# Optimization experiments

Measured on AMD Instinct MI355X. Metric: run time of the kernel, lower is better.

## Reference

```python
import jax, jax.numpy as jnp
import numpy as np

D_MODEL = 1024
N_HEADS = 16
HEAD_DIM = D_MODEL // N_HEADS


def setup_inputs() -> dict:
    key = jax.random.key(0)
    k1, k2, k3 = jax.random.split(key, 3)
    x = jax.random.normal(k1, (4, 2048, D_MODEL), dtype=jnp.float32)
    # torch Linear weight is [out, in]; y = x @ W.T
    w_qkv = jax.random.normal(k2, (3 * D_MODEL, D_MODEL), dtype=jnp.float32) * (1.0 / np.sqrt(D_MODEL))
    w_proj = jax.random.normal(k3, (D_MODEL, D_MODEL), dtype=jnp.float32) * (1.0 / np.sqrt(D_MODEL))
    return {"x": x, "w_qkv": w_qkv, "w_proj": w_proj}


def reference(x, w_qkv, w_proj):
    B, T, C = x.shape
    qkv = jnp.einsum('btc,oc->bto', x, w_qkv)  # [B,T,3C]
    q, k, v = jnp.split(qkv, 3, axis=-1)
    # [B,T,H,D] -> [B,H,T,D]
    def to_heads(t):
        return t.reshape(B, T, N_HEADS, HEAD_DIM).transpose(0, 2, 1, 3)
    q, k, v = to_heads(q), to_heads(k), to_heads(v)
    scale = 1.0 / np.sqrt(HEAD_DIM).astype(np.float32)
    scores = jnp.einsum('bhqd,bhkd->bhqk', q, k) * scale  # [B,H,T,T]
    causal = jnp.tril(jnp.ones((T, T), dtype=bool))
    scores = jnp.where(causal, scores, jnp.finfo(scores.dtype).min)
    attn = jax.nn.softmax(scores, axis=-1)
    out = jnp.einsum('bhqk,bhkd->bhqd', attn, v)  # [B,H,T,D]
    out = out.transpose(0, 2, 1, 3).reshape(B, T, C)
    return jnp.einsum('btc,oc->bto', out, w_proj)
```

## Files before the change

kernel.cpp:

```cpp
#include <hip/hip_runtime.h>

#define B_ 4
#define T_ 2048
#define C_ 1024
#define H_ 16
#define D_ 64

typedef __bf16 bf16;
typedef bf16 bf16x8 __attribute__((ext_vector_type(8)));
typedef bf16 bf16x4v __attribute__((ext_vector_type(4)));
typedef float f32x4 __attribute__((ext_vector_type(4)));

__device__ __forceinline__ int probe_is_f32(const void* p, int lane) {
  float v = fminf(fabsf((float)((const bf16*)p)[lane]), 100.f);
#pragma unroll
  for (int o = 1; o < 64; o <<= 1) v += __shfl_xor(v, o, 64);
  return v > 300.f ? 1 : 0;
}

__device__ __forceinline__ void gload16(const void* g, void* l) {
  __builtin_amdgcn_global_load_lds(
      (const __attribute__((address_space(1))) void*)g,
      (__attribute__((address_space(3))) void*)l, 16, 0, 0);
}

__global__ __launch_bounds__(256) void cvt_bf16(const void* __restrict__ src,
                                                bf16* __restrict__ dst,
                                                int n8) {
  if (!probe_is_f32(src, threadIdx.x & 63)) return;
  int i = blockIdx.x * 256 + threadIdx.x;
  if (i >= n8) return;
  const float* s = (const float*)src + (size_t)i * 8;
  f32x4 u0 = *(const f32x4*)s;
  f32x4 u1 = *(const f32x4*)(s + 4);
  bf16x8 o;
#pragma unroll
  for (int j = 0; j < 4; ++j) { o[j] = (bf16)u0[j]; o[4 + j] = (bf16)u1[j]; }
  *(bf16x8*)(dst + (size_t)i * 8) = o;
}

__global__ __launch_bounds__(256, 3) void gemm_bt(
    const void* __restrict__ A, const void* __restrict__ W,
    const bf16* __restrict__ Wcvt, int M, int N, int K, int amode, int omode,
    void* __restrict__ out, bf16* __restrict__ qb, bf16* __restrict__ kb,
    bf16* __restrict__ vtb, const void* __restrict__ px,
    const void* __restrict__ pwq, const void* __restrict__ pwp, int bsel) {
  __shared__ __align__(16) char lds[24576];
  char* ldsA = lds;
  char* ldsB = lds + 16384;

  const int ntiles = N >> 7;
  const int tm = blockIdx.x / ntiles;
  const int tn = blockIdx.x % ntiles;
  const int tid = threadIdx.x;
  const int lane = tid & 63;
  const int wv = tid >> 6;
  const int wm = wv >> 1, wn = wv & 1;
  const int lm = lane & 15, lq = lane >> 4;

  const int fx = probe_is_f32(px, lane);
  const int fwq = probe_is_f32(pwq, lane);
  const int fwp = probe_is_f32(pwp, lane);
  const int outF32 = fx | fwq | fwp;
  const int aF32 = (amode == 0) ? fx : 0;
  const int bF32 = bsel ? fwp : fwq;
  const bf16* Wb = bF32 ? Wcvt : (const bf16*)W;

  size_t boff[2];
#pragma unroll
  for (int h = 0; h < 2; ++h) {
    int c = tid + h * 256, rbk = c >> 6, ll = c & 63;
    boff[h] = (size_t)(tn * 128 + rbk * 16 + (ll & 15)) * K + (ll >> 4) * 8;
  }
  size_t aofff[4];
  size_t aoffb[2];
  int ab2[2], at2[2], acq[2];
  if (aF32) {
#pragma unroll
    for (int h = 0; h < 4; ++h) {
      int c = tid + h * 256, rb = c >> 7, w = c & 127;
      int q = w >> 5, lmm = (w >> 1) & 15, hf = w & 1;
      aofff[h] = (size_t)(tm * 128 + rb * 16 + lmm) * K + q * 8 + hf * 4;
    }
  } else {
#pragma unroll
    for (int h = 0; h < 2; ++h) {
      int c = tid + h * 256, rbk = c >> 6, ll = c & 63;
      int row = tm * 128 + rbk * 16 + (ll & 15);
      aoffb[h] = (size_t)row * K + (ll >> 4) * 8;
      ab2[h] = row >> 11;
      at2[h] = row & 2047;
      acq[h] = ll >> 4;
    }
  }

  f32x4 acc[4][4] = {};

  for (int k0 = 0; k0 < K; k0 += 32) {
    __syncthreads();
    if (aF32) {
#pragma unroll
      for (int h = 0; h < 4; ++h)
        gload16((const float*)A + aofff[h] + k0, ldsA + (tid + h * 256) * 16);
    } else if (amode == 2) {
#pragma unroll
      for (int h = 0; h < 2; ++h) {
        int kk = k0 + acq[h] * 8;
        size_t off =
            ((size_t)(ab2[h] * H_ + (kk >> 6)) * T_ + at2[h]) * D_ + (kk & 63);
        gload16((const bf16*)A + off, ldsA + (tid + h * 256) * 16);
      }
    } else {
#pragma unroll
      for (int h = 0; h < 2; ++h)
        gload16((const bf16*)A + aoffb[h] + k0, ldsA + (tid + h * 256) * 16);
    }
#pragma unroll
    for (int h = 0; h < 2; ++h)
      gload16(Wb + boff[h] + k0, ldsB + (tid + h * 256) * 16);
    __syncthreads();

    bf16x8 af[4], bff[4];
    if (aF32) {
#pragma unroll
      for (int i = 0; i < 4; ++i) {
        const char* p = ldsA + (wm * 4 + i) * 2048 + lane * 32;
        f32x4 u0 = *(const f32x4*)p;
        f32x4 u1 = *(const f32x4*)(p + 16);
#pragma unroll
        for (int j = 0; j < 4; ++j) {
          af[i][j] = (bf16)u0[j];
          af[i][4 + j] = (bf16)u1[j];
        }
      }
    } else {
#pragma unroll
      for (int i = 0; i < 4; ++i)
        af[i] = *(const bf16x8*)(ldsA + (wm * 4 + i) * 1024 + lane * 16);
    }
#pragma unroll
    for (int j = 0; j < 4; ++j)
      bff[j] = *(const bf16x8*)(ldsB + (wn * 4 + j) * 1024 + lane * 16);
#pragma unroll
    for (int i = 0; i < 4; ++i)
#pragma unroll
      for (int j = 0; j < 4; ++j)
        acc[i][j] = __builtin_amdgcn_mfma_f32_16x16x32_bf16(af[i], bff[j],
                                                            acc[i][j], 0, 0, 0);
  }

  if (omode == 0) {
#pragma unroll
    for (int i = 0; i < 4; ++i) {
      int row0 = tm * 128 + wm * 64 + i * 16 + lq * 4;
#pragma unroll
      for (int j = 0; j < 4; ++j) {
        int col = tn * 128 + wn * 64 + j * 16 + lm;
#pragma unroll
        for (int r = 0; r < 4; ++r) {
          size_t idx = (size_t)(row0 + r) * N + col;
          if (outF32) ((float*)out)[idx] = acc[i][j][r];
          else        ((bf16*)out)[idx]  = (bf16)acc[i][j][r];
        }
      }
    }
  } else {
#pragma unroll
    for (int j = 0; j < 4; ++j) {
      int o = tn * 128 + wn * 64 + j * 16 + lm;
      int which = o >> 10;
      int c = o & 1023;
      int h = c >> 6, d = c & 63;
#pragma unroll
      for (int i = 0; i < 4; ++i) {
        int row0 = tm * 128 + wm * 64 + i * 16 + lq * 4;
        int b = row0 >> 11, t0 = row0 & 2047;
        if (which == 2) {
          bf16x4v pk;
#pragma unroll
          for (int r = 0; r < 4; ++r) pk[r] = (bf16)acc[i][j][r];
          *(bf16x4v*)(vtb + ((size_t)((b * H_ + h) * D_ + d)) * T_ + t0) = pk;
        } else {
          bf16* dst = (which == 0) ? qb : kb;
#pragma unroll
          for (int r = 0; r < 4; ++r)
            dst[((size_t)((b * H_ + h) * T_ + t0 + r)) * D_ + d] =
                (bf16)acc[i][j][r];
        }
      }
    }
  }
}

__global__ __launch_bounds__(256, 4) void attn_fwd(bf16* __restrict__ Q,
                                                   const bf16* __restrict__ Kk,
                                                   const bf16* __restrict__ Vt) {
  __shared__ __align__(16) char lds[12288];
  char* ldsK = lds;
  char* ldsV = lds + 4096;
  char* ldsP = lds + 8192;

  const int tid = threadIdx.x;
  const int bh = blockIdx.x & 63;
  const int qt = blockIdx.x >> 6;
  const int lane = tid & 63;
  const int wv = tid >> 6;
  const int lm = lane & 15, lq = lane >> 4;
  const int q0w = qt * 64 + wv * 16;

  bf16x8 qa[2];
  {
    const bf16* qbase = Q + ((size_t)(bh * T_ + q0w + lm)) * D_ + lq * 8;
    qa[0] = *(const bf16x8*)(qbase);
    qa[1] = *(const bf16x8*)(qbase + 32);
  }

  const int kRow = (wv >> 1) * 16 + lm;
  const int kD = (wv & 1) * 32 + lq * 8;
  const int vD = wv * 16 + lm;

  const bf16* ksrc = Kk + ((size_t)(bh * T_ + kRow)) * D_ + kD;
  const bf16* vsrc = Vt + ((size_t)(bh * D_ + vD)) * T_ + lq * 8;

  f32x4 oacc[4] = {};
  float lsum[4] = {0.f, 0.f, 0.f, 0.f};
  char* myP = ldsP + wv * 1024;
  const int jend = qt * 64 + 64;

  for (int j0 = 0; j0 < jend; j0 += 32) {
    __syncthreads();
    gload16(ksrc + (size_t)j0 * D_, ldsK + tid * 16);
    gload16(vsrc + j0, ldsV + tid * 16);
    __syncthreads();

    bf16x8 kf[2][2], vf[4];
#pragma unroll
    for (int t = 0; t < 2; ++t)
#pragma unroll
      for (int kc = 0; kc < 2; ++kc)
        kf[t][kc] = *(const bf16x8*)(ldsK + (t * 2 + kc) * 1024 + lane * 16);
#pragma unroll
    for (int nt = 0; nt < 4; ++nt)
      vf[nt] = *(const bf16x8*)(ldsV + nt * 1024 + lane * 16);

#pragma unroll
    for (int t = 0; t < 2; ++t) {
      f32x4 s = {};
      s = __builtin_amdgcn_mfma_f32_16x16x32_bf16(qa[0], kf[t][0], s, 0, 0, 0);
      s = __builtin_amdgcn_mfma_f32_16x16x32_bf16(qa[1], kf[t][1], s, 0, 0, 0);
      int kcol = j0 + t * 16 + lm;
      int chunkc = t * 2 + (lm >> 3);
      int jj = lm & 7;
#pragma unroll
      for (int r = 0; r < 4; ++r) {
        int qrow = q0w + lq * 4 + r;
        float sc = fminf(fmaxf(s[r] * 0.125f, -30.f), 30.f);
        float p = (kcol <= qrow) ? __expf(sc) : 0.0f;
        bf16 pb = (bf16)p;
        lsum[r] += (float)pb;
        *(bf16*)(myP + (chunkc * 16 + lq * 4 + r) * 16 + jj * 2) = pb;
      }
    }
    bf16x8 pf = *(const bf16x8*)(myP + lane * 16);
#pragma unroll
    for (int nt = 0; nt < 4; ++nt)
      oacc[nt] = __builtin_amdgcn_mfma_f32_16x16x32_bf16(pf, vf[nt], oacc[nt],
                                                          0, 0, 0);
  }

  float rinv[4];
#pragma unroll
  for (int r = 0; r < 4; ++r) {
    float l = lsum[r];
    l += __shfl_xor(l, 1, 64);
    l += __shfl_xor(l, 2, 64);
    l += __shfl_xor(l, 4, 64);
    l += __shfl_xor(l, 8, 64);
    rinv[r] = 1.0f / fmaxf(l, 1e-30f);
  }
#pragma unroll
  for (int nt = 0; nt < 4; ++nt)
#pragma unroll
    for (int r = 0; r < 4; ++r) {
      int t = q0w + lq * 4 + r;
      Q[((size_t)(bh * T_ + t)) * D_ + nt * 16 + lm] =
          (bf16)(oacc[nt][r] * rinv[r]);
    }
}

extern "C" void kernel_launch(void* const* d_in, const int* in_sizes, int n_in,
                              void* d_out, int out_size, void* d_ws,
                              size_t ws_size, hipStream_t stream) {
  const void* x = d_in[0];
  const void* wqkv = d_in[1];
  const void* wproj = d_in[2];

  const size_t NE = (size_t)B_ * T_ * C_;
  bf16* qb = (bf16*)d_ws;
  bf16* kb = qb + NE;
  bf16* vtb = (bf16*)d_out;
  bf16* wqkvb = vtb + NE;
  bf16* wprojb = kb;

  const int M = B_ * T_;

  cvt_bf16<<<(3 * C_ * C_ / 8) / 256, 256, 0, stream>>>(wqkv, wqkvb,
                                                        3 * C_ * C_ / 8);
  gemm_bt<<<(M / 128) * (3 * C_ / 128), 256, 0, stream>>>(
      x, wqkv, wqkvb, M, 3 * C_, C_, 0, 1, nullptr, qb, kb,
      vtb, x, wqkv, wproj, 0);
  attn_fwd<<<(T_ / 64) * B_ * H_, 256, 0, stream>>>(qb, kb, vtb);
  cvt_bf16<<<(C_ * C_ / 8) / 256, 256, 0, stream>>>(wproj, wprojb,
                                                    C_ * C_ / 8);
  gemm_bt<<<(M / 128) * (C_ / 128), 256, 0, stream>>>(
      qb, wproj, wprojb, M, C_, C_, 2, 0, d_out, nullptr,
      nullptr, nullptr, x, wqkv, wproj, 1);
}
```

Baseline: 331.3 us.

## Pre-convert x to bf16 in halves and drop f32 A path from GEMM

Instead of loading fp32 activations into LDS and converting them inside the QKV GEMM, x is converted to bf16 in two halves by a separate kernel into a workspace buffer. The QKV GEMM is then launched twice, once per half of the rows, always reading bf16 A. This halves the A LDS footprint (24KB to 16KB), which may raise occupancy, and removes per-iteration conversion work. The cost is two extra conversion kernel launches and an extra round trip of x through memory, with staging space reused between halves.

```diff
diff --git a/kernel.cpp b/kernel.cpp
--- a/kernel.cpp
+++ b/kernel.cpp
@@ -25,12 +25,13 @@
 }
 
 __global__ __launch_bounds__(256) void cvt_bf16(const void* __restrict__ src,
+                                                size_t elofs,
                                                 bf16* __restrict__ dst,
                                                 int n8) {
   if (!probe_is_f32(src, threadIdx.x & 63)) return;
   int i = blockIdx.x * 256 + threadIdx.x;
   if (i >= n8) return;
-  const float* s = (const float*)src + (size_t)i * 8;
+  const float* s = (const float*)src + elofs + (size_t)i * 8;
   f32x4 u0 = *(const f32x4*)s;
   f32x4 u1 = *(const f32x4*)(s + 4);
   bf16x8 o;
@@ -40,17 +41,18 @@
 }
 
 __global__ __launch_bounds__(256, 3) void gemm_bt(
-    const void* __restrict__ A, const void* __restrict__ W,
-    const bf16* __restrict__ Wcvt, int M, int N, int K, int amode, int omode,
-    void* __restrict__ out, bf16* __restrict__ qb, bf16* __restrict__ kb,
-    bf16* __restrict__ vtb, const void* __restrict__ px,
-    const void* __restrict__ pwq, const void* __restrict__ pwp, int bsel) {
-  __shared__ __align__(16) char lds[24576];
+    const void* __restrict__ A, const bf16* __restrict__ Ab, int arowbase,
+    int tmofs, const void* __restrict__ W, const bf16* __restrict__ Wcvt,
+    int M, int N, int K, int amode, int omode, void* __restrict__ out,
+    bf16* __restrict__ qb, bf16* __restrict__ kb, bf16* __restrict__ vtb,
+    const void* __restrict__ px, const void* __restrict__ pwq,
+    const void* __restrict__ pwp, int bsel) {
+  __shared__ __align__(16) char lds[16384];
   char* ldsA = lds;
-  char* ldsB = lds + 16384;
+  char* ldsB = lds + 8192;
 
   const int ntiles = N >> 7;
-  const int tm = blockIdx.x / ntiles;
+  const int tm = tmofs + blockIdx.x / ntiles;
   const int tn = blockIdx.x % ntiles;
   const int tid = threadIdx.x;
   const int lane = tid & 63;
@@ -62,9 +64,10 @@
   const int fwq = probe_is_f32(pwq, lane);
   const int fwp = probe_is_f32(pwp, lane);
   const int outF32 = fx | fwq | fwp;
-  const int aF32 = (amode == 0) ? fx : 0;
   const int bF32 = bsel ? fwp : fwq;
   const bf16* Wb = bF32 ? Wcvt : (const bf16*)W;
+  const bf16* Asrc = (amode == 0 && fx) ? Ab : (const bf16*)A;
+  const int rowadj = (amode == 0 && fx) ? arowbase : 0;
 
   size_t boff[2];
 #pragma unroll
@@ -72,37 +75,23 @@
     int c = tid + h * 256, rbk = c >> 6, ll = c & 63;
     boff[h] = (size_t)(tn * 128 + rbk * 16 + (ll & 15)) * K + (ll >> 4) * 8;
   }
-  size_t aofff[4];
   size_t aoffb[2];
   int ab2[2], at2[2], acq[2];
-  if (aF32) {
-#pragma unroll
-    for (int h = 0; h < 4; ++h) {
-      int c = tid + h * 256, rb = c >> 7, w = c & 127;
-      int q = w >> 5, lmm = (w >> 1) & 15, hf = w & 1;
-      aofff[h] = (size_t)(tm * 128 + rb * 16 + lmm) * K + q * 8 + hf * 4;
-    }
-  } else {
-#pragma unroll
-    for (int h = 0; h < 2; ++h) {
-      int c = tid + h * 256, rbk = c >> 6, ll = c & 63;
-      int row = tm * 128 + rbk * 16 + (ll & 15);
-      aoffb[h] = (size_t)row * K + (ll >> 4) * 8;
-      ab2[h] = row >> 11;
-      at2[h] = row & 2047;
-      acq[h] = ll >> 4;
-    }
+#pragma unroll
+  for (int h = 0; h < 2; ++h) {
+    int c = tid + h * 256, rbk = c >> 6, ll = c & 63;
+    int row = tm * 128 + rbk * 16 + (ll & 15);
+    aoffb[h] = (size_t)(row - rowadj) * K + (ll >> 4) * 8;
+    ab2[h] = row >> 11;
+    at2[h] = row & 2047;
+    acq[h] = ll >> 4;
   }
 
   f32x4 acc[4][4] = {};
 
   for (int k0 = 0; k0 < K; k0 += 32) {
     __syncthreads();
-    if (aF32) {
-#pragma unroll
-      for (int h = 0; h < 4; ++h)
-        gload16((const float*)A + aofff[h] + k0, ldsA + (tid + h * 256) * 16);
-    } else if (amode == 2) {
+    if (amode == 2) {
 #pragma unroll
       for (int h = 0; h < 2; ++h) {
         int kk = k0 + acq[h] * 8;
@@ -113,7 +102,7 @@
     } else {
 #pragma unroll
       for (int h = 0; h < 2; ++h)
-        gload16((const bf16*)A + aoffb[h] + k0, ldsA + (tid + h * 256) * 16);
+        gload16(Asrc + aoffb[h] + k0, ldsA + (tid + h * 256) * 16);
     }
 #pragma unroll
     for (int h = 0; h < 2; ++h)
@@ -121,23 +110,9 @@
     __syncthreads();
 
     bf16x8 af[4], bff[4];
-    if (aF32) {
-#pragma unroll
-      for (int i = 0; i < 4; ++i) {
-        const char* p = ldsA + (wm * 4 + i) * 2048 + lane * 32;
-        f32x4 u0 = *(const f32x4*)p;
-        f32x4 u1 = *(const f32x4*)(p + 16);
-#pragma unroll
-        for (int j = 0; j < 4; ++j) {
-          af[i][j] = (bf16)u0[j];
-          af[i][4 + j] = (bf16)u1[j];
-        }
-      }
-    } else {
-#pragma unroll
-      for (int i = 0; i < 4; ++i)
-        af[i] = *(const bf16x8*)(ldsA + (wm * 4 + i) * 1024 + lane * 16);
-    }
+#pragma unroll
+    for (int i = 0; i < 4; ++i)
+      af[i] = *(const bf16x8*)(ldsA + (wm * 4 + i) * 1024 + lane * 16);
 #pragma unroll
     for (int j = 0; j < 4; ++j)
       bff[j] = *(const bf16x8*)(ldsB + (wn * 4 + j) * 1024 + lane * 16);
@@ -300,19 +275,29 @@
   bf16* kb = qb + NE;
   bf16* vtb = (bf16*)d_out;
   bf16* wqkvb = vtb + NE;
+  bf16* xb1 = wqkvb + 3 * C_ * C_;
   bf16* wprojb = kb;
 
   const int M = B_ * T_;
-
-  cvt_bf16<<<(3 * C_ * C_ / 8) / 256, 256, 0, stream>>>(wqkv, wqkvb,
+  const int Mh = M / 2;
+  const int nh8 = Mh * C_ / 8;
+
+  cvt_bf16<<<(3 * C_ * C_ / 8) / 256, 256, 0, stream>>>(wqkv, 0, wqkvb,
                                                         3 * C_ * C_ / 8);
-  gemm_bt<<<(M / 128) * (3 * C_ / 128), 256, 0, stream>>>(
-      x, wqkv, wqkvb, M, 3 * C_, C_, 0, 1, nullptr, qb, kb,
-      vtb, x, wqkv, wproj, 0);
+  cvt_bf16<<<nh8 / 256, 256, 0, stream>>>(x, 0, xb1, nh8);
+  gemm_bt<<<(Mh / 128) * (3 * C_ / 128), 256, 0, stream>>>(
+      x, xb1, 0, 0, wqkv, wqkvb, M, 3 * C_, C_,
+      0, 1, nullptr, qb, kb, vtb, x, wqkv, wproj,
+      0);
+  cvt_bf16<<<nh8 / 256, 256, 0, stream>>>(x, (size_t)Mh * C_, xb1, nh8);
+  gemm_bt<<<(Mh / 128) * (3 * C_ / 128), 256, 0, stream>>>(
+      x, xb1, Mh, Mh / 128, wqkv, wqkvb, M, 3 * C_, C_,
+      0, 1, nullptr, qb, kb, vtb, x, wqkv, wproj,
+      0);
   attn_fwd<<<(T_ / 64) * B_ * H_, 256, 0, stream>>>(qb, kb, vtb);
-  cvt_bf16<<<(C_ * C_ / 8) / 256, 256, 0, stream>>>(wproj, wprojb,
+  cvt_bf16<<<(C_ * C_ / 8) / 256, 256, 0, stream>>>(wproj, 0, wprojb,
                                                     C_ * C_ / 8);
   gemm_bt<<<(M / 128) * (C_ / 128), 256, 0, stream>>>(
-      qb, wproj, wprojb, M, C_, C_, 2, 0, d_out, nullptr,
-      nullptr, nullptr, x, wqkv, wproj, 1);
-}
+      qb, nullptr, 0, 0, wproj, wprojb, M, C_, C_, 2, 0,
+      d_out, nullptr, nullptr, nullptr, x, wqkv, wproj, 1);
+}
```

Measured after the change: 331.6 us. Within noise of the previous version (+0.1%).
